# Performance work log

Measured on AMD Instinct MI355X. Metric: run time of the kernel, lower is better.

The kernel has to match this reference:

```python
import jax, jax.numpy as jnp
import numpy as np

SCALE = 1.0 / np.sqrt(128.0).astype(np.float32)  # 1/sqrt(head_dim)


def setup_inputs() -> dict:
    key = jax.random.key(0)
    kq, kk, kv = jax.random.split(key, 3)
    B, S, D = 32, 2048, 128
    q = jax.random.normal(kq, (B, S, D), dtype=jnp.float32)
    k = jax.random.normal(kk, (B, S, D), dtype=jnp.float32)
    v = jax.random.normal(kv, (B, S, D), dtype=jnp.float32)
    return {"q": q, "k": k, "v": v}


def reference(q, k, v):
    # attention = bmm(q, k^T) * scale ; softmax over last (key) dim; bmm with v
    scores = jnp.einsum("bsd,btd->bst", q, k) * SCALE  # [B, S, S]
    attn = jax.nn.softmax(scores, axis=-1)
    return jnp.einsum("bst,btd->bsd", attn, v)  # [B, S, D]
```

## Files before the change

### kernel.cpp

```cpp
#include <hip/hip_runtime.h>
#include <math.h>
#include <stdint.h>

typedef __bf16 bf16_t;
typedef __bf16 bf16x2 __attribute__((ext_vector_type(2)));
typedef __bf16 bf16x4 __attribute__((ext_vector_type(4)));
typedef __bf16 bf16x8 __attribute__((ext_vector_type(8)));
typedef float f32x4 __attribute__((ext_vector_type(4)));

#define NB   32
#define SEQ  2048
#define HD   128
#define SCALE 0.08838834764831845f
#define LOG2E 1.4426950408889634f

__device__ __forceinline__ float fast_exp2(float x) {
#if __has_builtin(__builtin_amdgcn_exp2f)
  return __builtin_amdgcn_exp2f(x);
#else
  return exp2f(x);
#endif
}

__global__ __launch_bounds__(256) void prep_kernel(
    const float* __restrict__ Q, const float* __restrict__ K,
    const float* __restrict__ V, bf16_t* __restrict__ Qs,
    bf16_t* __restrict__ Kb, bf16_t* __restrict__ Vt)
{
  const int b = blockIdx.x;
  const int tid = threadIdx.x;
  if (b < 4096) {
    const bool isQ = (b < 2048);
    const float* src = isQ ? Q : K;
    bf16_t* dst = isQ ? Qs : Kb;
    const float sc = isQ ? (SCALE * LOG2E) : 1.0f;
    size_t base4 = (size_t)(isQ ? b : b - 2048) * 1024;
#pragma unroll
    for (int i = 0; i < 4; ++i) {
      size_t idx = base4 + tid + i * 256;
      float4 x = ((const float4*)src)[idx];
      bf16x4 y;
      y[0] = (bf16_t)(x.x * sc); y[1] = (bf16_t)(x.y * sc);
      y[2] = (bf16_t)(x.z * sc); y[3] = (bf16_t)(x.w * sc);
      ((bf16x4*)dst)[idx] = y;
    }
  } else {
    __shared__ float tile[64][65];
    const int bt = b - 4096;
    const int batch = bt >> 6;
    const int rem = bt & 63;
    const int s0 = (rem >> 1) * 64;
    const int d0 = (rem & 1) * 64;
#pragma unroll
    for (int i = 0; i < 4; ++i) {
      int e = tid + i * 256;
      int s = e >> 4, dq = e & 15;
      float4 x = *(const float4*)&V[((size_t)batch * SEQ + s0 + s) * HD + d0 + dq * 4];
      tile[s][dq * 4 + 0] = x.x;
      tile[s][dq * 4 + 1] = x.y;
      tile[s][dq * 4 + 2] = x.z;
      tile[s][dq * 4 + 3] = x.w;
    }
    __syncthreads();
#pragma unroll
    for (int i = 0; i < 2; ++i) {
      int g = tid + i * 256;
      int d = g >> 3, sg = g & 7;
      bf16x8 w;
#pragma unroll
      for (int j = 0; j < 8; ++j) w[j] = (bf16_t)tile[sg * 8 + j][d];
      *(bf16x8*)&Vt[((size_t)batch * HD + d0 + d) * SEQ + s0 + sg * 8] = w;
    }
  }
}

__global__ __launch_bounds__(256) void fa8_kernel(
    const bf16_t* __restrict__ Qs, const bf16_t* __restrict__ Kbf,
    const bf16_t* __restrict__ Vt, float* __restrict__ O)
{
  __shared__ __attribute__((aligned(16))) bf16_t Ksw[2][64 * 128];
  __shared__ __attribute__((aligned(16))) bf16_t Vsw[2][128 * 64];
  __shared__ __attribute__((aligned(16))) bf16_t Psh[4][16][72];

  const int tid  = threadIdx.x;
  const int lane = tid & 63;
  const int wq   = tid >> 6;
  const int quad = lane >> 4;
  const int l15  = lane & 15;

  const int batch = blockIdx.x >> 5;
  const int qt    = blockIdx.x & 31;

  const bf16_t* Qb = Qs + ((size_t)batch * SEQ + qt * 64) * HD;
  const bf16_t* Kb = Kbf + (size_t)batch * SEQ * HD;
  const bf16_t* Vb = Vt + (size_t)batch * HD * SEQ;
  float*        Ob = O + ((size_t)batch * SEQ + qt * 64) * HD;

  bf16x8 aq[4];
  {
    const int qrow = wq * 16 + l15;
#pragma unroll
    for (int kf = 0; kf < 4; ++kf)
      aq[kf] = *(const bf16x8*)&Qb[(size_t)qrow * HD + kf * 32 + quad * 8];
  }

  f32x4 o[8];
#pragma unroll
  for (int t = 0; t < 8; ++t) { o[t][0]=0.f; o[t][1]=0.f; o[t][2]=0.f; o[t][3]=0.f; }
  float m_r = -INFINITY, l_r = 0.0f;

  auto stage = [&](int buf, int kb) {
#pragma unroll
    for (int i = 0; i < 4; ++i) {
      int row = wq * 16 + i * 4 + (lane >> 4);
      int gk = (lane & 15) ^ (row & 15);
      const bf16_t* gp = Kb + (size_t)(kb + row) * HD + gk * 8;
      __builtin_amdgcn_global_load_lds(
          (const __attribute__((address_space(1))) void*)gp,
          (__attribute__((address_space(3))) void*)&Ksw[buf][(wq * 16 + i * 4) * 128],
          16, 0, 0);
    }
#pragma unroll
    for (int i = 0; i < 4; ++i) {
      int d = wq * 32 + i * 8 + (lane >> 3);
      int gv = (lane & 7) ^ (d & 7);
      const bf16_t* gp = Vb + (size_t)d * SEQ + kb + gv * 8;
      __builtin_amdgcn_global_load_lds(
          (const __attribute__((address_space(1))) void*)gp,
          (__attribute__((address_space(3))) void*)&Vsw[buf][(wq * 32 + i * 8) * 64],
          16, 0, 0);
    }
  };

  stage(0, 0);

  for (int it = 0; it < SEQ / 64; ++it) {
    __syncthreads();
    if (it + 1 < SEQ / 64) stage((it + 1) & 1, (it + 1) * 64);

    const bf16_t* Ks = &Ksw[it & 1][0];
    const bf16_t* Vs = &Vsw[it & 1][0];

    f32x4 s[4];
#pragma unroll
    for (int ct = 0; ct < 4; ++ct) { s[ct][0]=0.f; s[ct][1]=0.f; s[ct][2]=0.f; s[ct][3]=0.f; }
#pragma unroll
    for (int kf = 0; kf < 4; ++kf)
#pragma unroll
      for (int ct = 0; ct < 4; ++ct) {
        int row = ct * 16 + l15;
        bf16x8 ak = *(const bf16x8*)&Ks[row * 128 + (((kf * 4 + quad) ^ l15) * 8)];
        s[ct] = __builtin_amdgcn_mfma_f32_16x16x32_bf16(ak, aq[kf], s[ct], 0, 0, 0);
      }

    float mx = s[0][0];
#pragma unroll
    for (int ct = 0; ct < 4; ++ct)
#pragma unroll
      for (int r = 0; r < 4; ++r) mx = fmaxf(mx, s[ct][r]);
    mx = fmaxf(mx, __shfl_xor(mx, 16));
    mx = fmaxf(mx, __shfl_xor(mx, 32));

    if (!__all(mx <= m_r + 8.0f)) {
      const float mnew = fmaxf(m_r, mx);
      const float alpha = fast_exp2(m_r - mnew);
      m_r = mnew;
      l_r *= alpha;
#pragma unroll
      for (int t = 0; t < 8; ++t) {
        o[t][0]*=alpha; o[t][1]*=alpha; o[t][2]*=alpha; o[t][3]*=alpha;
      }
    }

    float ls = 0.f;
#pragma unroll
    for (int ct = 0; ct < 4; ++ct)
#pragma unroll
      for (int r = 0; r < 4; ++r) {
        float p = fast_exp2(s[ct][r] - m_r);
        s[ct][r] = p; ls += p;
      }
    ls += __shfl_xor(ls, 16);
    ls += __shfl_xor(ls, 32);
    l_r += ls;

#pragma unroll
    for (int ct = 0; ct < 4; ++ct) {
      bf16x4 pp;
      pp[0]=(bf16_t)s[ct][0]; pp[1]=(bf16_t)s[ct][1];
      pp[2]=(bf16_t)s[ct][2]; pp[3]=(bf16_t)s[ct][3];
      *(bf16x4*)&Psh[wq][l15][ct * 16 + quad * 4] = pp;
    }
    asm volatile("s_waitcnt lgkmcnt(0)" ::: "memory");
    bf16x8 ap0 = *(const bf16x8*)&Psh[wq][l15][quad * 8];
    bf16x8 ap1 = *(const bf16x8*)&Psh[wq][l15][32 + quad * 8];

#pragma unroll
    for (int t = 0; t < 8; ++t) {
      int d = t * 16 + l15;
      bf16x8 av0 = *(const bf16x8*)&Vs[d * 64 + ((quad ^ (l15 & 7)) * 8)];
      o[t] = __builtin_amdgcn_mfma_f32_16x16x32_bf16(av0, ap0, o[t], 0, 0, 0);
      bf16x8 av1 = *(const bf16x8*)&Vs[d * 64 + (((4 + quad) ^ (l15 & 7)) * 8)];
      o[t] = __builtin_amdgcn_mfma_f32_16x16x32_bf16(av1, ap1, o[t], 0, 0, 0);
    }
  }

  float inv = 1.0f / l_r;
  const int qrow = wq * 16 + l15;
#pragma unroll
  for (int t = 0; t < 8; ++t) {
    float4 w;
    w.x = o[t][0]*inv; w.y = o[t][1]*inv; w.z = o[t][2]*inv; w.w = o[t][3]*inv;
    *(float4*)&Ob[(size_t)qrow * HD + t * 16 + quad * 4] = w;
  }
}

#define BM   64
#define BN   64
#define KPAD 8
#define VPAD 8
#define PPAD 8

__global__ __launch_bounds__(256) void fa_fallback(
    const float* __restrict__ Q, const float* __restrict__ K,
    const float* __restrict__ V, float* __restrict__ O)
{
  __shared__ __attribute__((aligned(16))) bf16_t Ksh[BN][HD + KPAD];
  __shared__ __attribute__((aligned(16))) bf16_t Vsh[HD][BN + VPAD];
  __shared__ __attribute__((aligned(16))) bf16_t Psh[4][16][BN + PPAD];

  const int tid = threadIdx.x;
  const int lane = tid & 63;
  const int wq = tid >> 6;
  const int quad = lane >> 4;
  const int l15 = lane & 15;
  const int bid = blockIdx.x;
  const int batch = bid >> 5;
  const int qt = bid & 31;

  const float* Qb = Q + (size_t)batch * SEQ * HD + (size_t)qt * BM * HD;
  const float* Kb = K + (size_t)batch * SEQ * HD;
  const float* Vb = V + (size_t)batch * SEQ * HD;
  float* Ob = O + (size_t)batch * SEQ * HD + (size_t)qt * BM * HD;

  bf16x8 aq[4];
  {
    const int qrow = wq * 16 + l15;
#pragma unroll
    for (int kf = 0; kf < 4; ++kf) {
      const float* qp = Qb + (size_t)qrow * HD + kf * 32 + quad * 8;
      float4 x0 = *(const float4*)(qp);
      float4 x1 = *(const float4*)(qp + 4);
      bf16x8 a;
      a[0] = (bf16_t)(x0.x * SCALE); a[1] = (bf16_t)(x0.y * SCALE);
      a[2] = (bf16_t)(x0.z * SCALE); a[3] = (bf16_t)(x0.w * SCALE);
      a[4] = (bf16_t)(x1.x * SCALE); a[5] = (bf16_t)(x1.y * SCALE);
      a[6] = (bf16_t)(x1.z * SCALE); a[7] = (bf16_t)(x1.w * SCALE);
      aq[kf] = a;
    }
  }

  f32x4 o[8];
#pragma unroll
  for (int t = 0; t < 8; ++t) { o[t][0]=0.f; o[t][1]=0.f; o[t][2]=0.f; o[t][3]=0.f; }
  float m_r = -INFINITY, l_r = 0.0f;
  const int vkp = (tid & 31) * 2;
  const int vg = tid >> 5;
  float4 kreg[8], vreg[8];

#pragma unroll
  for (int i = 0; i < 8; ++i) {
    int v = tid + i * 256, row = v >> 5, c4 = (v & 31) * 4;
    kreg[i] = *(const float4*)(Kb + (size_t)row * HD + c4);
  }
#pragma unroll
  for (int i = 0; i < 4; ++i) {
    int d0 = (vg + i * 8) * 4;
    const float* vp0 = Vb + (size_t)vkp * HD + d0;
    vreg[2 * i] = *(const float4*)vp0;
    vreg[2 * i + 1] = *(const float4*)(vp0 + HD);
  }

  for (int kb = 0; kb < SEQ; kb += BN) {
    __syncthreads();
#pragma unroll
    for (int i = 0; i < 8; ++i) {
      int v = tid + i * 256, row = v >> 5, c4 = (v & 31) * 4;
      float4 kv = kreg[i];
      bf16x4 kk;
      kk[0]=(bf16_t)kv.x; kk[1]=(bf16_t)kv.y; kk[2]=(bf16_t)kv.z; kk[3]=(bf16_t)kv.w;
      *(bf16x4*)&Ksh[row][c4] = kk;
    }
#pragma unroll
    for (int i = 0; i < 4; ++i) {
      int d0 = (vg + i * 8) * 4;
      float4 a0 = vreg[2 * i], a1 = vreg[2 * i + 1];
      bf16x2 p0; p0[0]=(bf16_t)a0.x; p0[1]=(bf16_t)a1.x;
      bf16x2 p1; p1[0]=(bf16_t)a0.y; p1[1]=(bf16_t)a1.y;
      bf16x2 p2; p2[0]=(bf16_t)a0.z; p2[1]=(bf16_t)a1.z;
      bf16x2 p3; p3[0]=(bf16_t)a0.w; p3[1]=(bf16_t)a1.w;
      *(bf16x2*)&Vsh[d0 + 0][vkp] = p0;
      *(bf16x2*)&Vsh[d0 + 1][vkp] = p1;
      *(bf16x2*)&Vsh[d0 + 2][vkp] = p2;
      *(bf16x2*)&Vsh[d0 + 3][vkp] = p3;
    }
    __syncthreads();

    const int kbn = kb + BN;
    if (kbn < SEQ) {
#pragma unroll
      for (int i = 0; i < 8; ++i) {
        int v = tid + i * 256, row = v >> 5, c4 = (v & 31) * 4;
        kreg[i] = *(const float4*)(Kb + (size_t)(kbn + row) * HD + c4);
      }
#pragma unroll
      for (int i = 0; i < 4; ++i) {
        int d0 = (vg + i * 8) * 4;
        const float* vp0 = Vb + (size_t)(kbn + vkp) * HD + d0;
        vreg[2 * i] = *(const float4*)vp0;
        vreg[2 * i + 1] = *(const float4*)(vp0 + HD);
      }
    }

    f32x4 s[4];
#pragma unroll
    for (int ct = 0; ct < 4; ++ct) { s[ct][0]=0.f; s[ct][1]=0.f; s[ct][2]=0.f; s[ct][3]=0.f; }
#pragma unroll
    for (int kf = 0; kf < 4; ++kf)
#pragma unroll
      for (int ct = 0; ct < 4; ++ct) {
        bf16x8 ak = *(const bf16x8*)&Ksh[ct * 16 + l15][kf * 32 + quad * 8];
        s[ct] = __builtin_amdgcn_mfma_f32_16x16x32_bf16(ak, aq[kf], s[ct], 0, 0, 0);
      }

    float mx = s[0][0];
#pragma unroll
    for (int ct = 0; ct < 4; ++ct)
#pragma unroll
      for (int r = 0; r < 4; ++r) mx = fmaxf(mx, s[ct][r]);
    mx = fmaxf(mx, __shfl_xor(mx, 16));
    mx = fmaxf(mx, __shfl_xor(mx, 32));
    float mnew = fmaxf(m_r, mx);
    float alpha = __expf(m_r - mnew);
    m_r = mnew;
    float ls = 0.f;
#pragma unroll
    for (int ct = 0; ct < 4; ++ct)
#pragma unroll
      for (int r = 0; r < 4; ++r) {
        float p = __expf(s[ct][r] - mnew);
        s[ct][r] = p; ls += p;
      }
    ls += __shfl_xor(ls, 16);
    ls += __shfl_xor(ls, 32);
    l_r = l_r * alpha + ls;

#pragma unroll
    for (int ct = 0; ct < 4; ++ct) {
      bf16x4 pp;
      pp[0]=(bf16_t)s[ct][0]; pp[1]=(bf16_t)s[ct][1];
      pp[2]=(bf16_t)s[ct][2]; pp[3]=(bf16_t)s[ct][3];
      *(bf16x4*)&Psh[wq][l15][ct * 16 + quad * 4] = pp;
    }
    asm volatile("s_waitcnt lgkmcnt(0)" ::: "memory");
    bf16x8 ap0 = *(const bf16x8*)&Psh[wq][l15][quad * 8];
    bf16x8 ap1 = *(const bf16x8*)&Psh[wq][l15][32 + quad * 8];

#pragma unroll
    for (int t = 0; t < 8; ++t) {
      o[t][0]*=alpha; o[t][1]*=alpha; o[t][2]*=alpha; o[t][3]*=alpha;
    }
#pragma unroll
    for (int t = 0; t < 8; ++t) {
      bf16x8 av0 = *(const bf16x8*)&Vsh[t * 16 + l15][quad * 8];
      o[t] = __builtin_amdgcn_mfma_f32_16x16x32_bf16(av0, ap0, o[t], 0, 0, 0);
      bf16x8 av1 = *(const bf16x8*)&Vsh[t * 16 + l15][32 + quad * 8];
      o[t] = __builtin_amdgcn_mfma_f32_16x16x32_bf16(av1, ap1, o[t], 0, 0, 0);
    }
  }

  float inv = 1.0f / l_r;
  const int qrow = wq * 16 + l15;
#pragma unroll
  for (int t = 0; t < 8; ++t) {
    float4 w;
    w.x = o[t][0]*inv; w.y = o[t][1]*inv; w.z = o[t][2]*inv; w.w = o[t][3]*inv;
    *(float4*)&Ob[(size_t)qrow * HD + t * 16 + quad * 4] = w;
  }
}

extern "C" void kernel_launch(void* const* d_in, const int* in_sizes, int n_in,
                              void* d_out, int out_size, void* d_ws, size_t ws_size,
                              hipStream_t stream) {
  const float* q = (const float*)d_in[0];
  const float* k = (const float*)d_in[1];
  const float* v = (const float*)d_in[2];
  float* out = (float*)d_out;

  const size_t elems = (size_t)NB * SEQ * HD;
  const size_t need = elems * 2 * 3;

  if (ws_size >= need) {
    bf16_t* Qs = (bf16_t*)d_ws;
    bf16_t* Kb = Qs + elems;
    bf16_t* Vt = Kb + elems;
    prep_kernel<<<6144, 256, 0, stream>>>(q, k, v, Qs, Kb, Vt);
    fa8_kernel<<<NB * (SEQ / 64), 256, 0, stream>>>(Qs, Kb, Vt, out);
  } else {
    fa_fallback<<<NB * (SEQ / BM), 256, 0, stream>>>(q, k, v, out);
  }
}
```

Before: 251.7 us.

## Software-pipeline PV matmul one tile behind and shuffle P through registers

Defers the P·V MFMA for tile t-1 until after the QK^T MFMAs of tile t, so softmax work for one tile can overlap matrix work from the previous one. A third V buffer in shared memory and rotating pointers keep the previous V tile resident while the next one is prefetched. The P transpose that went through per-wave shared memory is replaced by bf16-pair packing and cross-lane __shfl, removing LDS stores, a waitcnt and reloads. The cost is more shared memory, a drain step after the loop, and extra shuffle instructions and register pressure.

Result: slower. 258.7 us (+2.8%).

```diff
diff --git a/kernel.cpp b/kernel.cpp
--- a/kernel.cpp
+++ b/kernel.cpp
@@ -74,13 +74,12 @@
   }
 }
 
-__global__ __launch_bounds__(256) void fa8_kernel(
+__global__ __launch_bounds__(256) void fa9_kernel(
     const bf16_t* __restrict__ Qs, const bf16_t* __restrict__ Kbf,
     const bf16_t* __restrict__ Vt, float* __restrict__ O)
 {
   __shared__ __attribute__((aligned(16))) bf16_t Ksw[2][64 * 128];
-  __shared__ __attribute__((aligned(16))) bf16_t Vsw[2][128 * 64];
-  __shared__ __attribute__((aligned(16))) bf16_t Psh[4][16][72];
+  __shared__ __attribute__((aligned(16))) bf16_t Vsw[3][128 * 64];
 
   const int tid  = threadIdx.x;
   const int lane = tid & 63;
@@ -109,7 +108,9 @@
   for (int t = 0; t < 8; ++t) { o[t][0]=0.f; o[t][1]=0.f; o[t][2]=0.f; o[t][3]=0.f; }
   float m_r = -INFINITY, l_r = 0.0f;
 
-  auto stage = [&](int buf, int kb) {
+  bf16x8 ap0p, ap1p;
+
+  auto stage = [&](int kbuf, bf16_t* vdst, int kb) {
 #pragma unroll
     for (int i = 0; i < 4; ++i) {
       int row = wq * 16 + i * 4 + (lane >> 4);
@@ -117,7 +118,7 @@
       const bf16_t* gp = Kb + (size_t)(kb + row) * HD + gk * 8;
       __builtin_amdgcn_global_load_lds(
           (const __attribute__((address_space(1))) void*)gp,
-          (__attribute__((address_space(3))) void*)&Ksw[buf][(wq * 16 + i * 4) * 128],
+          (__attribute__((address_space(3))) void*)&Ksw[kbuf][(wq * 16 + i * 4) * 128],
           16, 0, 0);
     }
 #pragma unroll
@@ -127,19 +128,22 @@
       const bf16_t* gp = Vb + (size_t)d * SEQ + kb + gv * 8;
       __builtin_amdgcn_global_load_lds(
           (const __attribute__((address_space(1))) void*)gp,
-          (__attribute__((address_space(3))) void*)&Vsw[buf][(wq * 32 + i * 8) * 64],
+          (__attribute__((address_space(3))) void*)&(vdst[(wq * 32 + i * 8) * 64]),
           16, 0, 0);
     }
   };
 
-  stage(0, 0);
-
-  for (int it = 0; it < SEQ / 64; ++it) {
+  bf16_t* vA = &Vsw[0][0];
+  bf16_t* vB = &Vsw[1][0];
+  bf16_t* vC = &Vsw[2][0];
+
+  stage(0, vA, 0);
+
+  for (int t = 0; t < SEQ / 64; ++t) {
     __syncthreads();
-    if (it + 1 < SEQ / 64) stage((it + 1) & 1, (it + 1) * 64);
-
-    const bf16_t* Ks = &Ksw[it & 1][0];
-    const bf16_t* Vs = &Vsw[it & 1][0];
+    if (t < SEQ / 64 - 1) stage((t + 1) & 1, vB, (t + 1) * 64);
+
+    const bf16_t* Ks = &Ksw[t & 1][0];
 
     f32x4 s[4];
 #pragma unroll
@@ -153,11 +157,22 @@
         s[ct] = __builtin_amdgcn_mfma_f32_16x16x32_bf16(ak, aq[kf], s[ct], 0, 0, 0);
       }
 
-    float mx = s[0][0];
-#pragma unroll
-    for (int ct = 0; ct < 4; ++ct)
-#pragma unroll
-      for (int r = 0; r < 4; ++r) mx = fmaxf(mx, s[ct][r]);
+    if (t > 0) {
+#pragma unroll
+      for (int tt = 0; tt < 8; ++tt) {
+        int d = tt * 16 + l15;
+        bf16x8 a0 = *(const bf16x8*)&vC[d * 64 + ((quad ^ (l15 & 7)) * 8)];
+        o[tt] = __builtin_amdgcn_mfma_f32_16x16x32_bf16(a0, ap0p, o[tt], 0, 0, 0);
+        bf16x8 a1 = *(const bf16x8*)&vC[d * 64 + (((4 + quad) ^ (l15 & 7)) * 8)];
+        o[tt] = __builtin_amdgcn_mfma_f32_16x16x32_bf16(a1, ap1p, o[tt], 0, 0, 0);
+      }
+    }
+
+    float m01a = fmaxf(fmaxf(s[0][0], s[0][1]), fmaxf(s[0][2], s[0][3]));
+    float m01b = fmaxf(fmaxf(s[1][0], s[1][1]), fmaxf(s[1][2], s[1][3]));
+    float m23a = fmaxf(fmaxf(s[2][0], s[2][1]), fmaxf(s[2][2], s[2][3]));
+    float m23b = fmaxf(fmaxf(s[3][0], s[3][1]), fmaxf(s[3][2], s[3][3]));
+    float mx = fmaxf(fmaxf(m01a, m01b), fmaxf(m23a, m23b));
     mx = fmaxf(mx, __shfl_xor(mx, 16));
     mx = fmaxf(mx, __shfl_xor(mx, 32));
 
@@ -167,42 +182,63 @@
       m_r = mnew;
       l_r *= alpha;
 #pragma unroll
-      for (int t = 0; t < 8; ++t) {
-        o[t][0]*=alpha; o[t][1]*=alpha; o[t][2]*=alpha; o[t][3]*=alpha;
+      for (int tt = 0; tt < 8; ++tt) {
+        o[tt][0]*=alpha; o[tt][1]*=alpha; o[tt][2]*=alpha; o[tt][3]*=alpha;
       }
     }
 
     float ls = 0.f;
 #pragma unroll
-    for (int ct = 0; ct < 4; ++ct)
-#pragma unroll
-      for (int r = 0; r < 4; ++r) {
-        float p = fast_exp2(s[ct][r] - m_r);
-        s[ct][r] = p; ls += p;
-      }
+    for (int ct = 0; ct < 4; ++ct) {
+      float p0 = fast_exp2(s[ct][0] - m_r);
+      float p1 = fast_exp2(s[ct][1] - m_r);
+      float p2 = fast_exp2(s[ct][2] - m_r);
+      float p3 = fast_exp2(s[ct][3] - m_r);
+      s[ct][0] = p0; s[ct][1] = p1; s[ct][2] = p2; s[ct][3] = p3;
+      ls += (p0 + p1) + (p2 + p3);
+    }
     ls += __shfl_xor(ls, 16);
     ls += __shfl_xor(ls, 32);
     l_r += ls;
 
-#pragma unroll
-    for (int ct = 0; ct < 4; ++ct) {
-      bf16x4 pp;
-      pp[0]=(bf16_t)s[ct][0]; pp[1]=(bf16_t)s[ct][1];
-      pp[2]=(bf16_t)s[ct][2]; pp[3]=(bf16_t)s[ct][3];
-      *(bf16x4*)&Psh[wq][l15][ct * 16 + quad * 4] = pp;
-    }
-    asm volatile("s_waitcnt lgkmcnt(0)" ::: "memory");
-    bf16x8 ap0 = *(const bf16x8*)&Psh[wq][l15][quad * 8];
-    bf16x8 ap1 = *(const bf16x8*)&Psh[wq][l15][32 + quad * 8];
-
-#pragma unroll
-    for (int t = 0; t < 8; ++t) {
-      int d = t * 16 + l15;
-      bf16x8 av0 = *(const bf16x8*)&Vs[d * 64 + ((quad ^ (l15 & 7)) * 8)];
-      o[t] = __builtin_amdgcn_mfma_f32_16x16x32_bf16(av0, ap0, o[t], 0, 0, 0);
-      bf16x8 av1 = *(const bf16x8*)&Vs[d * 64 + (((4 + quad) ^ (l15 & 7)) * 8)];
-      o[t] = __builtin_amdgcn_mfma_f32_16x16x32_bf16(av1, ap1, o[t], 0, 0, 0);
-    }
+    int pk[4][2];
+#pragma unroll
+    for (int ct = 0; ct < 4; ++ct)
+#pragma unroll
+      for (int h = 0; h < 2; ++h) {
+        union { bf16x2 v; int u; } c;
+        c.v[0] = (bf16_t)s[ct][2 * h];
+        c.v[1] = (bf16_t)s[ct][2 * h + 1];
+        pk[ct][h] = c.u;
+      }
+    {
+      const int srcA = l15 + ((quad & 1) << 5);
+      const int srcB = srcA + 16;
+      union { bf16x8 v; int w[4]; } A0, A1;
+#pragma unroll
+      for (int w = 0; w < 4; ++w) {
+        const int src = (w >> 1) ? srcB : srcA;
+        int x0 = __shfl(pk[0][w & 1], src);
+        int x1 = __shfl(pk[1][w & 1], src);
+        int y0 = __shfl(pk[2][w & 1], src);
+        int y1 = __shfl(pk[3][w & 1], src);
+        A0.w[w] = (quad >> 1) ? x1 : x0;
+        A1.w[w] = (quad >> 1) ? y1 : y0;
+      }
+      ap0p = A0.v;
+      ap1p = A1.v;
+    }
+
+    bf16_t* tmp = vC; vC = vA; vA = vB; vB = tmp;
+  }
+
+#pragma unroll
+  for (int tt = 0; tt < 8; ++tt) {
+    int d = tt * 16 + l15;
+    bf16x8 a0 = *(const bf16x8*)&vC[d * 64 + ((quad ^ (l15 & 7)) * 8)];
+    o[tt] = __builtin_amdgcn_mfma_f32_16x16x32_bf16(a0, ap0p, o[tt], 0, 0, 0);
+    bf16x8 a1 = *(const bf16x8*)&vC[d * 64 + (((4 + quad) ^ (l15 & 7)) * 8)];
+    o[tt] = __builtin_amdgcn_mfma_f32_16x16x32_bf16(a1, ap1p, o[tt], 0, 0, 0);
   }
 
   float inv = 1.0f / l_r;
@@ -405,7 +441,7 @@
     bf16_t* Kb = Qs + elems;
     bf16_t* Vt = Kb + elems;
     prep_kernel<<<6144, 256, 0, stream>>>(q, k, v, Qs, Kb, Vt);
-    fa8_kernel<<<NB * (SEQ / 64), 256, 0, stream>>>(Qs, Kb, Vt, out);
+    fa9_kernel<<<NB * (SEQ / 64), 256, 0, stream>>>(Qs, Kb, Vt, out);
   } else {
     fa_fallback<<<NB * (SEQ / BM), 256, 0, stream>>>(q, k, v, out);
   }
```

## Load V fragments directly from global into registers, drop V LDS staging

Applied to the files above, without the earlier changes.

V tiles are no longer staged through shared memory with global_load_lds. Each wave now loads its V MFMA operands straight from global memory into registers at the top of each iteration, and only K stays double-buffered in LDS. The change also adds a launch bound of 3 blocks per CU, relying on the halved LDS footprint to allow more resident blocks. The trade-offs are that every wave redundantly fetches the same V data through L2/L1, the added register pressure could cause spills under the occupancy hint, and global load latency is now only hidden by the QK^T compute.

New measurement: 389.4 us. +54.7%, slower.

```diff
diff --git a/kernel.cpp b/kernel.cpp
--- a/kernel.cpp
+++ b/kernel.cpp
@@ -74,12 +74,11 @@
   }
 }
 
-__global__ __launch_bounds__(256) void fa8_kernel(
+__global__ __launch_bounds__(256, 3) void fa10_kernel(
     const bf16_t* __restrict__ Qs, const bf16_t* __restrict__ Kbf,
     const bf16_t* __restrict__ Vt, float* __restrict__ O)
 {
   __shared__ __attribute__((aligned(16))) bf16_t Ksw[2][64 * 128];
-  __shared__ __attribute__((aligned(16))) bf16_t Vsw[2][128 * 64];
   __shared__ __attribute__((aligned(16))) bf16_t Psh[4][16][72];
 
   const int tid  = threadIdx.x;
@@ -109,7 +108,7 @@
   for (int t = 0; t < 8; ++t) { o[t][0]=0.f; o[t][1]=0.f; o[t][2]=0.f; o[t][3]=0.f; }
   float m_r = -INFINITY, l_r = 0.0f;
 
-  auto stage = [&](int buf, int kb) {
+  auto stageK = [&](int buf, int kb) {
 #pragma unroll
     for (int i = 0; i < 4; ++i) {
       int row = wq * 16 + i * 4 + (lane >> 4);
@@ -120,26 +119,25 @@
           (__attribute__((address_space(3))) void*)&Ksw[buf][(wq * 16 + i * 4) * 128],
           16, 0, 0);
     }
-#pragma unroll
-    for (int i = 0; i < 4; ++i) {
-      int d = wq * 32 + i * 8 + (lane >> 3);
-      int gv = (lane & 7) ^ (d & 7);
-      const bf16_t* gp = Vb + (size_t)d * SEQ + kb + gv * 8;
-      __builtin_amdgcn_global_load_lds(
-          (const __attribute__((address_space(1))) void*)gp,
-          (__attribute__((address_space(3))) void*)&Vsw[buf][(wq * 32 + i * 8) * 64],
-          16, 0, 0);
-    }
   };
 
-  stage(0, 0);
-
-  for (int it = 0; it < SEQ / 64; ++it) {
+  stageK(0, 0);
+
+  for (int t = 0; t < SEQ / 64; ++t) {
     __syncthreads();
-    if (it + 1 < SEQ / 64) stage((it + 1) & 1, (it + 1) * 64);
-
-    const bf16_t* Ks = &Ksw[it & 1][0];
-    const bf16_t* Vs = &Vsw[it & 1][0];
+    const int kb = t * 64;
+
+    bf16x8 av0[8], av1[8];
+#pragma unroll
+    for (int tt = 0; tt < 8; ++tt) {
+      const bf16_t* vp = Vb + (size_t)(tt * 16 + l15) * SEQ + kb;
+      av0[tt] = *(const bf16x8*)&vp[quad * 8];
+      av1[tt] = *(const bf16x8*)&vp[32 + quad * 8];
+    }
+
+    if (t + 1 < SEQ / 64) stageK((t + 1) & 1, (t + 1) * 64);
+
+    const bf16_t* Ks = &Ksw[t & 1][0];
 
     f32x4 s[4];
 #pragma unroll
@@ -167,8 +165,8 @@
       m_r = mnew;
       l_r *= alpha;
 #pragma unroll
-      for (int t = 0; t < 8; ++t) {
-        o[t][0]*=alpha; o[t][1]*=alpha; o[t][2]*=alpha; o[t][3]*=alpha;
+      for (int tt = 0; tt < 8; ++tt) {
+        o[tt][0]*=alpha; o[tt][1]*=alpha; o[tt][2]*=alpha; o[tt][3]*=alpha;
       }
     }
 
@@ -196,12 +194,9 @@
     bf16x8 ap1 = *(const bf16x8*)&Psh[wq][l15][32 + quad * 8];
 
 #pragma unroll
-    for (int t = 0; t < 8; ++t) {
-      int d = t * 16 + l15;
-      bf16x8 av0 = *(const bf16x8*)&Vs[d * 64 + ((quad ^ (l15 & 7)) * 8)];
-      o[t] = __builtin_amdgcn_mfma_f32_16x16x32_bf16(av0, ap0, o[t], 0, 0, 0);
-      bf16x8 av1 = *(const bf16x8*)&Vs[d * 64 + (((4 + quad) ^ (l15 & 7)) * 8)];
-      o[t] = __builtin_amdgcn_mfma_f32_16x16x32_bf16(av1, ap1, o[t], 0, 0, 0);
+    for (int tt = 0; tt < 8; ++tt) {
+      o[tt] = __builtin_amdgcn_mfma_f32_16x16x32_bf16(av0[tt], ap0, o[tt], 0, 0, 0);
+      o[tt] = __builtin_amdgcn_mfma_f32_16x16x32_bf16(av1[tt], ap1, o[tt], 0, 0, 0);
     }
   }
 
@@ -405,7 +400,7 @@
     bf16_t* Kb = Qs + elems;
     bf16_t* Vt = Kb + elems;
     prep_kernel<<<6144, 256, 0, stream>>>(q, k, v, Qs, Kb, Vt);
-    fa8_kernel<<<NB * (SEQ / 64), 256, 0, stream>>>(Qs, Kb, Vt, out);
+    fa10_kernel<<<NB * (SEQ / 64), 256, 0, stream>>>(Qs, Kb, Vt, out);
   } else {
     fa_fallback<<<NB * (SEQ / BM), 256, 0, stream>>>(q, k, v, out);
   }
```

## Switch attention to 32x32 MFMA with split-key waves and register-shuffled P

Applied to the files above, without the earlier changes.

Rewrites the flash-attention inner loop to use 32x32x16 bf16 MFMA. Each pair of waves shares 32 query rows and splits every 64-key tile into two 32-key halves. The P matrix is passed between half-waves with lane shuffles instead of a shared-memory round trip, and the two partial softmax states are merged through LDS in an epilogue. The aim is fewer MFMA issues, fewer LDS reads per FLOP and no LDS traffic for P. The cost is extra epilogue synchronisation, a merge step, and higher register pressure from the 16-wide accumulators.

Measured after the change: 238.5 us. 1.06x faster.

```diff
diff --git a/kernel.cpp b/kernel.cpp
--- a/kernel.cpp
+++ b/kernel.cpp
@@ -7,6 +7,7 @@
 typedef __bf16 bf16x4 __attribute__((ext_vector_type(4)));
 typedef __bf16 bf16x8 __attribute__((ext_vector_type(8)));
 typedef float f32x4 __attribute__((ext_vector_type(4)));
+typedef float f32x16 __attribute__((ext_vector_type(16)));
 
 #define NB   32
 #define SEQ  2048
@@ -74,39 +75,41 @@
   }
 }
 
-__global__ __launch_bounds__(256) void fa8_kernel(
+__global__ __launch_bounds__(256) void fa12_kernel(
     const bf16_t* __restrict__ Qs, const bf16_t* __restrict__ Kbf,
     const bf16_t* __restrict__ Vt, float* __restrict__ O)
 {
   __shared__ __attribute__((aligned(16))) bf16_t Ksw[2][64 * 128];
   __shared__ __attribute__((aligned(16))) bf16_t Vsw[2][128 * 64];
-  __shared__ __attribute__((aligned(16))) bf16_t Psh[4][16][72];
+  __shared__ float mlbuf[2][2][32];
 
   const int tid  = threadIdx.x;
   const int lane = tid & 63;
   const int wq   = tid >> 6;
-  const int quad = lane >> 4;
-  const int l15  = lane & 15;
+  const int hi   = lane >> 5;
+  const int q31  = lane & 31;
+  const int pair = wq >> 1;
+  const int sub  = wq & 1;
+  const int koff = sub * 32;
 
   const int batch = blockIdx.x >> 5;
   const int qt    = blockIdx.x & 31;
 
-  const bf16_t* Qb = Qs + ((size_t)batch * SEQ + qt * 64) * HD;
+  const bf16_t* Qb = Qs + ((size_t)batch * SEQ + qt * 64 + pair * 32) * HD;
   const bf16_t* Kb = Kbf + (size_t)batch * SEQ * HD;
   const bf16_t* Vb = Vt + (size_t)batch * HD * SEQ;
   float*        Ob = O + ((size_t)batch * SEQ + qt * 64) * HD;
 
-  bf16x8 aq[4];
-  {
-    const int qrow = wq * 16 + l15;
-#pragma unroll
-    for (int kf = 0; kf < 4; ++kf)
-      aq[kf] = *(const bf16x8*)&Qb[(size_t)qrow * HD + kf * 32 + quad * 8];
-  }
-
-  f32x4 o[8];
-#pragma unroll
-  for (int t = 0; t < 8; ++t) { o[t][0]=0.f; o[t][1]=0.f; o[t][2]=0.f; o[t][3]=0.f; }
+  bf16x8 bq[8];
+#pragma unroll
+  for (int dc = 0; dc < 8; ++dc)
+    bq[dc] = *(const bf16x8*)&Qb[(size_t)q31 * HD + dc * 16 + hi * 8];
+
+  f32x16 o[4];
+#pragma unroll
+  for (int dt = 0; dt < 4; ++dt)
+#pragma unroll
+    for (int r = 0; r < 16; ++r) o[dt][r] = 0.f;
   float m_r = -INFINITY, l_r = 0.0f;
 
   auto stage = [&](int buf, int kb) {
@@ -134,31 +137,29 @@
 
   stage(0, 0);
 
-  for (int it = 0; it < SEQ / 64; ++it) {
+  for (int t = 0; t < SEQ / 64; ++t) {
     __syncthreads();
-    if (it + 1 < SEQ / 64) stage((it + 1) & 1, (it + 1) * 64);
-
-    const bf16_t* Ks = &Ksw[it & 1][0];
-    const bf16_t* Vs = &Vsw[it & 1][0];
-
-    f32x4 s[4];
-#pragma unroll
-    for (int ct = 0; ct < 4; ++ct) { s[ct][0]=0.f; s[ct][1]=0.f; s[ct][2]=0.f; s[ct][3]=0.f; }
-#pragma unroll
-    for (int kf = 0; kf < 4; ++kf)
-#pragma unroll
-      for (int ct = 0; ct < 4; ++ct) {
-        int row = ct * 16 + l15;
-        bf16x8 ak = *(const bf16x8*)&Ks[row * 128 + (((kf * 4 + quad) ^ l15) * 8)];
-        s[ct] = __builtin_amdgcn_mfma_f32_16x16x32_bf16(ak, aq[kf], s[ct], 0, 0, 0);
-      }
-
-    float mx = s[0][0];
-#pragma unroll
-    for (int ct = 0; ct < 4; ++ct)
-#pragma unroll
-      for (int r = 0; r < 4; ++r) mx = fmaxf(mx, s[ct][r]);
-    mx = fmaxf(mx, __shfl_xor(mx, 16));
+    if (t + 1 < SEQ / 64) stage((t + 1) & 1, (t + 1) * 64);
+
+    const bf16_t* Ks = &Ksw[t & 1][0];
+    const bf16_t* Vs = &Vsw[t & 1][0];
+
+    f32x16 s;
+#pragma unroll
+    for (int r = 0; r < 16; ++r) s[r] = 0.f;
+    {
+      const int row = koff + q31;
+      const int rsw = row & 15;
+#pragma unroll
+      for (int dc = 0; dc < 8; ++dc) {
+        bf16x8 ak = *(const bf16x8*)&Ks[row * 128 + (((dc * 2 + hi) ^ rsw) * 8)];
+        s = __builtin_amdgcn_mfma_f32_32x32x16_bf16(ak, bq[dc], s, 0, 0, 0);
+      }
+    }
+
+    float mx = s[0];
+#pragma unroll
+    for (int r = 1; r < 16; ++r) mx = fmaxf(mx, s[r]);
     mx = fmaxf(mx, __shfl_xor(mx, 32));
 
     if (!__all(mx <= m_r + 8.0f)) {
@@ -167,51 +168,100 @@
       m_r = mnew;
       l_r *= alpha;
 #pragma unroll
-      for (int t = 0; t < 8; ++t) {
-        o[t][0]*=alpha; o[t][1]*=alpha; o[t][2]*=alpha; o[t][3]*=alpha;
-      }
+      for (int dt = 0; dt < 4; ++dt) o[dt] = o[dt] * alpha;
     }
 
     float ls = 0.f;
 #pragma unroll
-    for (int ct = 0; ct < 4; ++ct)
-#pragma unroll
-      for (int r = 0; r < 4; ++r) {
-        float p = fast_exp2(s[ct][r] - m_r);
-        s[ct][r] = p; ls += p;
-      }
-    ls += __shfl_xor(ls, 16);
+    for (int r = 0; r < 16; ++r) {
+      float p = fast_exp2(s[r] - m_r);
+      s[r] = p; ls += p;
+    }
     ls += __shfl_xor(ls, 32);
     l_r += ls;
 
-#pragma unroll
-    for (int ct = 0; ct < 4; ++ct) {
-      bf16x4 pp;
-      pp[0]=(bf16_t)s[ct][0]; pp[1]=(bf16_t)s[ct][1];
-      pp[2]=(bf16_t)s[ct][2]; pp[3]=(bf16_t)s[ct][3];
-      *(bf16x4*)&Psh[wq][l15][ct * 16 + quad * 4] = pp;
-    }
-    asm volatile("s_waitcnt lgkmcnt(0)" ::: "memory");
-    bf16x8 ap0 = *(const bf16x8*)&Psh[wq][l15][quad * 8];
-    bf16x8 ap1 = *(const bf16x8*)&Psh[wq][l15][32 + quad * 8];
-
-#pragma unroll
-    for (int t = 0; t < 8; ++t) {
-      int d = t * 16 + l15;
-      bf16x8 av0 = *(const bf16x8*)&Vs[d * 64 + ((quad ^ (l15 & 7)) * 8)];
-      o[t] = __builtin_amdgcn_mfma_f32_16x16x32_bf16(av0, ap0, o[t], 0, 0, 0);
-      bf16x8 av1 = *(const bf16x8*)&Vs[d * 64 + (((4 + quad) ^ (l15 & 7)) * 8)];
-      o[t] = __builtin_amdgcn_mfma_f32_16x16x32_bf16(av1, ap1, o[t], 0, 0, 0);
-    }
-  }
-
-  float inv = 1.0f / l_r;
-  const int qrow = wq * 16 + l15;
-#pragma unroll
-  for (int t = 0; t < 8; ++t) {
-    float4 w;
-    w.x = o[t][0]*inv; w.y = o[t][1]*inv; w.z = o[t][2]*inv; w.w = o[t][3]*inv;
-    *(float4*)&Ob[(size_t)qrow * HD + t * 16 + quad * 4] = w;
+    uint32_t pk[8];
+#pragma unroll
+    for (int i = 0; i < 8; ++i) {
+      union { bf16x2 v; uint32_t u; } c;
+      c.v[0] = (bf16_t)s[2 * i];
+      c.v[1] = (bf16_t)s[2 * i + 1];
+      pk[i] = c.u;
+    }
+    uint32_t t0 = __shfl_xor((int)(hi ? pk[0] : pk[2]), 32);
+    uint32_t t1 = __shfl_xor((int)(hi ? pk[1] : pk[3]), 32);
+    uint32_t t2 = __shfl_xor((int)(hi ? pk[4] : pk[6]), 32);
+    uint32_t t3 = __shfl_xor((int)(hi ? pk[5] : pk[7]), 32);
+    bf16x8 bp0, bp1;
+    {
+      union { bf16x8 v; uint32_t w[4]; } B;
+      if (hi) { B.w[0] = t0; B.w[1] = t1; B.w[2] = pk[2]; B.w[3] = pk[3]; }
+      else    { B.w[0] = pk[0]; B.w[1] = pk[1]; B.w[2] = t0; B.w[3] = t1; }
+      bp0 = B.v;
+      if (hi) { B.w[0] = t2; B.w[1] = t3; B.w[2] = pk[6]; B.w[3] = pk[7]; }
+      else    { B.w[0] = pk[4]; B.w[1] = pk[5]; B.w[2] = t2; B.w[3] = t3; }
+      bp1 = B.v;
+    }
+
+    {
+      const int g0 = (koff >> 3) + hi;
+      const int g1 = g0 + 2;
+#pragma unroll
+      for (int dt = 0; dt < 4; ++dt) {
+        const int d = dt * 32 + q31;
+        const int dsw = d & 7;
+        bf16x8 av0 = *(const bf16x8*)&Vs[d * 64 + ((g0 ^ dsw) * 8)];
+        o[dt] = __builtin_amdgcn_mfma_f32_32x32x16_bf16(av0, bp0, o[dt], 0, 0, 0);
+        bf16x8 av1 = *(const bf16x8*)&Vs[d * 64 + ((g1 ^ dsw) * 8)];
+        o[dt] = __builtin_amdgcn_mfma_f32_32x32x16_bf16(av1, bp1, o[dt], 0, 0, 0);
+      }
+    }
+  }
+
+  __syncthreads();
+  float* obuf = (pair == 0) ? (float*)&Ksw[0][0] : (float*)&Vsw[0][0];
+
+  if (sub == 1) {
+    if (hi == 0) {
+      mlbuf[pair][0][q31] = m_r;
+      mlbuf[pair][1][q31] = l_r;
+    }
+#pragma unroll
+    for (int dt = 0; dt < 4; ++dt)
+#pragma unroll
+      for (int r = 0; r < 16; ++r) {
+        int d = dt * 32 + (r & 3) + 8 * (r >> 2) + 4 * hi;
+        obuf[q31 * 132 + d] = o[dt][r];
+      }
+  }
+  __syncthreads();
+  if (sub == 0) {
+    float m1 = mlbuf[pair][0][q31];
+    float l1 = mlbuf[pair][1][q31];
+    float m = fmaxf(m_r, m1);
+    float e0 = fast_exp2(m_r - m);
+    float e1 = fast_exp2(m1 - m);
+    float inv = 1.0f / (l_r * e0 + l1 * e1);
+    float f0 = e0 * inv, f1 = e1 * inv;
+#pragma unroll
+    for (int dt = 0; dt < 4; ++dt)
+#pragma unroll
+      for (int r = 0; r < 16; ++r) {
+        int d = dt * 32 + (r & 3) + 8 * (r >> 2) + 4 * hi;
+        obuf[q31 * 132 + d] = o[dt][r] * f0 + obuf[q31 * 132 + d] * f1;
+      }
+  }
+  __syncthreads();
+  {
+    const int tid2 = sub * 64 + lane;
+#pragma unroll
+    for (int i = 0; i < 8; ++i) {
+      int idx = tid2 + i * 128;
+      int q = idx >> 5;
+      int dg = idx & 31;
+      float4 v = *(const float4*)&obuf[q * 132 + dg * 4];
+      *(float4*)&Ob[(size_t)(pair * 32 + q) * HD + dg * 4] = v;
+    }
   }
 }
 
@@ -405,7 +455,7 @@
     bf16_t* Kb = Qs + elems;
     bf16_t* Vt = Kb + elems;
     prep_kernel<<<6144, 256, 0, stream>>>(q, k, v, Qs, Kb, Vt);
-    fa8_kernel<<<NB * (SEQ / 64), 256, 0, stream>>>(Qs, Kb, Vt, out);
+    fa12_kernel<<<NB * (SEQ / 64), 256, 0, stream>>>(Qs, Kb, Vt, out);
   } else {
     fa_fallback<<<NB * (SEQ / BM), 256, 0, stream>>>(q, k, v, out);
   }
```
